# Optimization experiments

Hardware: AMD Instinct MI355X
Metric: run time of the kernel (lower is better)

Reference implementation:

```python
import jax, jax.numpy as jnp
import numpy as np

NUM_HEADS = 16

def _w8a8_linear(x_q, x_scale, w_q, w_scale, bias):
    # W8A8 GEMM with dynamic per-token input scale and per-output-channel weight scale
    # x_q: [N, Din] int8 values, w_q: [Dout, Din] int8 values
    acc = jnp.matmul(x_q.astype(jnp.float32), w_q.astype(jnp.float32).T)  # [N, Dout]
    return acc * (x_scale[:, None] * w_scale[None, :]) + bias[None, :]


def setup_inputs() -> dict:
    key = jax.random.key(0)
    ks = jax.random.split(key, 16)
    B, S, D = 2, 2048, 1024
    N = B * S
    def int8(k, shape):
        return jax.random.randint(k, shape, -127, 128, dtype=jnp.int32)
    inp = {
        "x_q": int8(ks[0], (N, D)),
        "x_scale": jax.random.uniform(ks[1], (N,), jnp.float32, 0.005, 0.02),
        "wq": int8(ks[2], (D, D)),
        "wq_scale": jax.random.uniform(ks[3], (D,), jnp.float32, 0.005, 0.02),
        "bq": jax.random.normal(ks[4], (D,), jnp.float32) * 0.02,
        "wk": int8(ks[5], (D, D)),
        "wk_scale": jax.random.uniform(ks[6], (D,), jnp.float32, 0.005, 0.02),
        "bk": jax.random.normal(ks[7], (D,), jnp.float32) * 0.02,
        "wv": int8(ks[8], (D, D)),
        "wv_scale": jax.random.uniform(ks[9], (D,), jnp.float32, 0.005, 0.02),
        "bv": jax.random.normal(ks[10], (D,), jnp.float32) * 0.02,
        "wo": int8(ks[11], (D, D)),
        "wo_scale": jax.random.uniform(ks[12], (D,), jnp.float32, 0.005, 0.02),
        "bo": jax.random.normal(ks[13], (D,), jnp.float32) * 0.02,
        "bsz": B,
        "qlen": S,
    }
    return inp


def reference(x_q, x_scale, wq, wq_scale, bq, wk, wk_scale, bk,
              wv, wv_scale, bv, wo, wo_scale, bo, bsz, qlen):
    D = wq.shape[0]
    hd = D // NUM_HEADS
    # quantized QKV projections (dequant fused into GEMM epilogue)
    q = _w8a8_linear(x_q, x_scale, wq, wq_scale, bq).reshape(bsz, qlen, NUM_HEADS, hd)
    k = _w8a8_linear(x_q, x_scale, wk, wk_scale, bk).reshape(bsz, qlen, NUM_HEADS, hd)
    v = _w8a8_linear(x_q, x_scale, wv, wv_scale, bv).reshape(bsz, qlen, NUM_HEADS, hd)
    # flash_attn_func(softmax_scale=None, causal=False) => scale = 1/sqrt(head_dim)
    scale = 1.0 / jnp.sqrt(jnp.float32(hd))
    scores = jnp.einsum('bqhd,bkhd->bhqk', q, k) * scale
    probs = jax.nn.softmax(scores, axis=-1)
    attn = jnp.einsum('bhqk,bkhd->bqhd', probs, v).reshape(bsz * qlen, D)
    # invoke_quant: dynamic per-token symmetric int8 quantization of attn output
    o_scale = jnp.max(jnp.abs(attn), axis=-1) / 127.0  # [N]
    o_q = jnp.clip(jnp.round(attn / o_scale[:, None]), -127.0, 127.0)
    # quantized out projection
    out = _w8a8_linear(o_q, o_scale, wo, wo_scale, bo)  # [N, D]
    return out
```

## Files before the change

kernel.cpp:

```cpp
#include <hip/hip_runtime.h>

#define D_MODEL 1024
#define NTOK    4096
#define SEQ     2048
#define NH      16
#define HD      64

typedef __bf16 bh8  __attribute__((ext_vector_type(8)));
typedef __bf16 bf4  __attribute__((ext_vector_type(4)));
typedef float  f32x4 __attribute__((ext_vector_type(4)));
typedef int    i32x4 __attribute__((ext_vector_type(4)));

__device__ __forceinline__ unsigned short f2bf(float f) {
  unsigned int u = __float_as_uint(f);
  u += 0x7fffu + ((u >> 16) & 1u);
  return (unsigned short)(u >> 16);
}
__device__ __forceinline__ float bf2f(unsigned short h) {
  return __uint_as_float(((unsigned int)h) << 16);
}
__device__ __forceinline__ float exp2a(float x) {
  float r; asm("v_exp_f32 %0, %1" : "=v"(r) : "v"(x)); return r;
}
__device__ __forceinline__ void gl16(const void* g, void* l) {
  __builtin_amdgcn_global_load_lds((const __attribute__((address_space(1))) unsigned int*)g,
                                   (__attribute__((address_space(3))) unsigned int*)l, 16, 0, 0);
}

__device__ __forceinline__ void pack_row(const int* src, unsigned* dst, int m, int t) {
  int4 w = *(const int4*)(src + (size_t)m * 1024 + t * 4);
  unsigned p01 = __builtin_amdgcn_perm((unsigned)w.y, (unsigned)w.x, 0x00000400u);
  unsigned p23 = __builtin_amdgcn_perm((unsigned)w.w, (unsigned)w.z, 0x00000400u);
  unsigned r   = __builtin_amdgcn_perm(p23, p01, 0x05040100u);
  int kg = t >> 4, c = (t >> 2) & 3, b4 = t & 3, sw = (m >> 1) & 3;
  dst[(size_t)m * 256 + kg * 16 + ((c ^ sw) << 2) + b4] = r;
}
__launch_bounds__(256)
__global__ void pack_x_k(const int* __restrict__ src, unsigned* __restrict__ dst) {
  pack_row(src, dst, blockIdx.x, threadIdx.x);
}
__launch_bounds__(256)
__global__ void pack_w_k(const int* __restrict__ s0, const int* __restrict__ s1,
                         const int* __restrict__ s2, const int* __restrict__ s3,
                         unsigned* __restrict__ d0, unsigned* __restrict__ d1,
                         unsigned* __restrict__ d2, unsigned* __restrict__ d3) {
  int wsel = blockIdx.x >> 10, m = blockIdx.x & 1023;
  const int* src = wsel == 0 ? s0 : wsel == 1 ? s1 : wsel == 2 ? s2 : s3;
  unsigned*  dst = wsel == 0 ? d0 : wsel == 1 ? d1 : wsel == 2 ? d2 : d3;
  pack_row(src, dst, m, threadIdx.x);
}

template <int MODE>
__launch_bounds__(256, 2)
__global__ void gemm8_k(const signed char* __restrict__ Ap, const signed char* __restrict__ Bp,
                        const float* __restrict__ sA, const float* __restrict__ sB,
                        const float* __restrict__ bias, float preScale, int kswz,
                        unsigned short* __restrict__ o1, unsigned short* __restrict__ o2,
                        float* __restrict__ outF)
{
  __shared__ __align__(16) signed char As[2][8192];
  __shared__ __align__(16) signed char Bs[2][8192];
  const int t = threadIdx.x, wid = t >> 6, lane = t & 63, g = lane >> 4, li = lane & 15;
  const int wm = wid >> 1, wn = wid & 1;
  const int m0 = blockIdx.y * 128, n0 = blockIdx.x * 128;

  i32x4 acc[4][4];
#pragma unroll
  for (int i = 0; i < 4; ++i)
#pragma unroll
    for (int j = 0; j < 4; ++j) acc[i][j] = (i32x4){0, 0, 0, 0};

  const int unitBase = wid * 2;
#pragma unroll
  for (int i = 0; i < 2; ++i) {
    int unit = (unitBase + i) * 64 + lane, r = unit >> 2, c = unit & 3;
    gl16(Ap + (size_t)(m0 + r) * 1024 + c * 16, (char*)As[0] + (unitBase + i) * 1024);
    gl16(Bp + (size_t)(n0 + r) * 1024 + c * 16, (char*)Bs[0] + (unitBase + i) * 1024);
  }
  __syncthreads();
  int p = 0;
#pragma unroll 1
  for (int ks = 0; ks < 16; ++ks) {
    if (ks < 15) {
      const int k0 = (ks + 1) * 64;
#pragma unroll
      for (int i = 0; i < 2; ++i) {
        int unit = (unitBase + i) * 64 + lane, r = unit >> 2, c = unit & 3;
        gl16(Ap + (size_t)(m0 + r) * 1024 + k0 + c * 16, (char*)As[p ^ 1] + (unitBase + i) * 1024);
        gl16(Bp + (size_t)(n0 + r) * 1024 + k0 + c * 16, (char*)Bs[p ^ 1] + (unitBase + i) * 1024);
      }
    }
    i32x4 af[4], bfr[4];
#pragma unroll
    for (int mt = 0; mt < 4; ++mt) {
      int row = wm * 64 + mt * 16 + li;
      af[mt] = *(const i32x4*)(As[p] + row * 64 + ((g ^ ((row >> 1) & 3)) << 4));
    }
#pragma unroll
    for (int nt = 0; nt < 4; ++nt) {
      int row = wn * 64 + nt * 16 + li;
      bfr[nt] = *(const i32x4*)(Bs[p] + row * 64 + ((g ^ ((row >> 1) & 3)) << 4));
    }
    __builtin_amdgcn_s_setprio(1);
#pragma unroll
    for (int mt = 0; mt < 4; ++mt)
#pragma unroll
      for (int nt = 0; nt < 4; ++nt)
        acc[mt][nt] = __builtin_amdgcn_mfma_i32_16x16x64_i8(af[mt], bfr[nt], acc[mt][nt], 0, 0, 0);
    __builtin_amdgcn_s_setprio(0);
    __syncthreads();
    p ^= 1;
  }

#pragma unroll
  for (int mt = 0; mt < 4; ++mt) {
#pragma unroll
    for (int nt = 0; nt < 4; ++nt) {
      const int nn = n0 + wn * 64 + nt * 16 + li;
#pragma unroll
      for (int r = 0; r < 4; ++r) {
        const int m = m0 + wm * 64 + mt * 16 + g * 4 + r;
        const float a = (float)acc[mt][nt][r];
        if (MODE == 0) {
          float f = (a * (sA[m] * sB[nn]) + bias[nn]) * preScale;
          int bb = m >> 11, s = m & 2047, hh = nn >> 6, d = nn & 63;
          int dd = kswz ? ((((d >> 3) ^ (s & 7)) << 3) | (d & 7)) : d;
          size_t o = (((size_t)(bb * NH + hh)) * SEQ + s) * HD + dd;
          unsigned short hi = f2bf(f);
          unsigned short lo = f2bf(f - bf2f(hi));
          o1[o] = hi; o2[o] = lo;
        } else if (MODE == 2) {
          float f = a * (sA[m] * sB[nn]) + bias[m];
          int hh = m >> 6, d = m & 63, bb = nn >> 11, s = nn & 2047;
          int ss = (s & ~63) | (((((s >> 3) & 7) ^ (d & 7)) << 3) | (s & 7));
          size_t o = (((size_t)(bb * NH + hh)) * HD + d) * SEQ + ss;
          o1[o] = f2bf(f);
        } else {
          outF[(size_t)m * 1024 + nn] = a * (sA[m] * sB[nn]) + bias[nn];
        }
      }
    }
  }
}

__launch_bounds__(256, 2)
__global__ void attn_k(const unsigned short* __restrict__ qhi, const unsigned short* __restrict__ qlo,
                       const unsigned short* __restrict__ khi, const unsigned short* __restrict__ klo,
                       const unsigned short* __restrict__ vt, float* __restrict__ attn)
{
  __shared__ __align__(16) unsigned short khs[64 * 64], kls[64 * 64], vts[64 * 64];
  __shared__ __align__(16) unsigned short ps[4][16 * 64];
  const int t = threadIdx.x;
  const int w = t >> 6, lane = t & 63, g = lane >> 4, li = lane & 15;
  const int q0 = blockIdx.x * 64, h = blockIdx.y, b = blockIdx.z;
  const int bh = b * NH + h;

  const unsigned short* qrh = qhi + ((size_t)bh * SEQ + q0 + w * 16 + li) * HD;
  const unsigned short* qrl = qlo + ((size_t)bh * SEQ + q0 + w * 16 + li) * HD;
  bh8 qhf[2], qlf[2];
#pragma unroll
  for (int kc = 0; kc < 2; ++kc) {
    qhf[kc] = *(const bh8*)(qrh + kc * 32 + g * 8);
    qlf[kc] = *(const bh8*)(qrl + kc * 32 + g * 8);
  }
  const unsigned short* kb = khi + (size_t)bh * SEQ * HD;
  const unsigned short* lb = klo + (size_t)bh * SEQ * HD;
  const unsigned short* vb = vt  + (size_t)bh * HD * SEQ;

  float m_run = -INFINITY, l_run = 0.0f;
  f32x4 ot[4];
#pragma unroll
  for (int i = 0; i < 4; ++i) ot[i] = (f32x4)0.0f;

  for (int kk0 = 0; kk0 < SEQ; kk0 += 64) {
    __syncthreads();
#pragma unroll
    for (int i = 0; i < 2; ++i) {
      int unit = (w * 2 + i) * 64 + lane, r = unit >> 3, c = unit & 7;
      gl16(kb + (size_t)(kk0 + r) * 64 + c * 8, (char*)khs + (w * 2 + i) * 1024);
      gl16(lb + (size_t)(kk0 + r) * 64 + c * 8, (char*)kls + (w * 2 + i) * 1024);
      gl16(vb + (size_t)r * SEQ + kk0 + c * 8, (char*)vts + (w * 2 + i) * 1024);
    }
    __syncthreads();

    f32x4 sa[4];
#pragma unroll
    for (int kt2 = 0; kt2 < 4; ++kt2) {
      sa[kt2] = (f32x4)0.0f;
      int row = kt2 * 16 + li, rx = row & 7;
#pragma unroll
      for (int kc = 0; kc < 2; ++kc) {
        bh8 kh = *(const bh8*)((const char*)khs + row * 128 + ((((kc << 2) | g) ^ rx) << 4));
        bh8 kl = *(const bh8*)((const char*)kls + row * 128 + ((((kc << 2) | g) ^ rx) << 4));
        __builtin_amdgcn_s_setprio(1);
        sa[kt2] = __builtin_amdgcn_mfma_f32_16x16x32_bf16(kh, qhf[kc], sa[kt2], 0, 0, 0);
        sa[kt2] = __builtin_amdgcn_mfma_f32_16x16x32_bf16(kh, qlf[kc], sa[kt2], 0, 0, 0);
        sa[kt2] = __builtin_amdgcn_mfma_f32_16x16x32_bf16(kl, qhf[kc], sa[kt2], 0, 0, 0);
        __builtin_amdgcn_s_setprio(0);
      }
    }
    float p[4][4];
    float sm = -INFINITY;
#pragma unroll
    for (int kt2 = 0; kt2 < 4; ++kt2)
#pragma unroll
      for (int r = 0; r < 4; ++r) { p[kt2][r] = sa[kt2][r]; sm = fmaxf(sm, p[kt2][r]); }
    sm = fmaxf(sm, __shfl_xor(sm, 16));
    sm = fmaxf(sm, __shfl_xor(sm, 32));
    if (__any(sm > m_run + 11.0f)) {
      float mn = fmaxf(m_run, sm);
      float alpha = exp2a(m_run - mn);
      l_run *= alpha;
#pragma unroll
      for (int i = 0; i < 4; ++i) ot[i] *= alpha;
      m_run = mn;
    }
    float ts = 0.0f;
#pragma unroll
    for (int kt2 = 0; kt2 < 4; ++kt2)
#pragma unroll
      for (int r = 0; r < 4; ++r) { float e = exp2a(p[kt2][r] - m_run); p[kt2][r] = e; ts += e; }
    ts += __shfl_xor(ts, 16);
    ts += __shfl_xor(ts, 32);
    l_run += ts;

#pragma unroll
    for (int kt2 = 0; kt2 < 4; ++kt2) {
      bf4 pk = { (__bf16)p[kt2][0], (__bf16)p[kt2][1], (__bf16)p[kt2][2], (__bf16)p[kt2][3] };
      int lchunk = (kt2 << 1) | (g >> 1);
      *(bf4*)((char*)ps[w] + li * 128 + ((lchunk ^ (li & 7)) << 4) + ((g & 1) << 3)) = pk;
    }
    asm volatile("s_waitcnt lgkmcnt(0)" ::: "memory");
    __builtin_amdgcn_sched_barrier(0);

#pragma unroll
    for (int kc2 = 0; kc2 < 2; ++kc2) {
      bh8 pf = *(const bh8*)((const char*)ps[w] + li * 128 + ((((kc2 << 2) | g) ^ (li & 7)) << 4));
#pragma unroll
      for (int dt = 0; dt < 4; ++dt) {
        int rowd = dt * 16 + li;
        bh8 vf = *(const bh8*)((const char*)vts + rowd * 128 + ((((kc2 << 2) | g) ^ (rowd & 7)) << 4));
        __builtin_amdgcn_s_setprio(1);
        ot[dt] = __builtin_amdgcn_mfma_f32_16x16x32_bf16(vf, pf, ot[dt], 0, 0, 0);
        __builtin_amdgcn_s_setprio(0);
      }
    }
  }

  const float inv = 1.0f / l_run;
  const int n = b * SEQ + q0 + w * 16 + li;
#pragma unroll
  for (int dt = 0; dt < 4; ++dt) {
    float4 o4;
    o4.x = ot[dt][0] * inv; o4.y = ot[dt][1] * inv;
    o4.z = ot[dt][2] * inv; o4.w = ot[dt][3] * inv;
    *(float4*)(attn + (size_t)n * D_MODEL + h * HD + dt * 16 + g * 4) = o4;
  }
}

__launch_bounds__(256)
__global__ void quant_k(const float* __restrict__ attn, unsigned* __restrict__ oqp,
                        float* __restrict__ osc)
{
  const int row = blockIdx.x, t = threadIdx.x;
  float4 v = *(const float4*)(attn + (size_t)row * D_MODEL + t * 4);
  float mx = fmaxf(fmaxf(fabsf(v.x), fabsf(v.y)), fmaxf(fabsf(v.z), fabsf(v.w)));
#pragma unroll
  for (int off = 1; off < 64; off <<= 1) mx = fmaxf(mx, __shfl_xor(mx, off));
  __shared__ float red[4];
  if ((t & 63) == 0) red[t >> 6] = mx;
  __syncthreads();
  mx = fmaxf(fmaxf(red[0], red[1]), fmaxf(red[2], red[3]));
  const float s = mx / 127.0f;
  if (t == 0) osc[row] = s;
  int q0 = (int)fminf(fmaxf(rintf(v.x / s), -127.f), 127.f);
  int q1 = (int)fminf(fmaxf(rintf(v.y / s), -127.f), 127.f);
  int q2 = (int)fminf(fmaxf(rintf(v.z / s), -127.f), 127.f);
  int q3 = (int)fminf(fmaxf(rintf(v.w / s), -127.f), 127.f);
  unsigned pk = ((unsigned)q0 & 255u) | (((unsigned)q1 & 255u) << 8) |
                (((unsigned)q2 & 255u) << 16) | (((unsigned)q3 & 255u) << 24);
  int kg = t >> 4, c = (t >> 2) & 3, b4 = t & 3, sw = (row >> 1) & 3;
  oqp[(size_t)row * 256 + kg * 16 + ((c ^ sw) << 2) + b4] = pk;
}

extern "C" void kernel_launch(void* const* d_in, const int* in_sizes, int n_in,
                              void* d_out, int out_size, void* d_ws, size_t ws_size,
                              hipStream_t stream)
{
  const int*   x   = (const int*)d_in[0];
  const float* xs  = (const float*)d_in[1];
  const int*   wq  = (const int*)d_in[2];
  const float* wqs = (const float*)d_in[3];
  const float* bq  = (const float*)d_in[4];
  const int*   wk  = (const int*)d_in[5];
  const float* wks = (const float*)d_in[6];
  const float* bk  = (const float*)d_in[7];
  const int*   wv  = (const int*)d_in[8];
  const float* wvs = (const float*)d_in[9];
  const float* bv  = (const float*)d_in[10];
  const int*   wo  = (const int*)d_in[11];
  const float* wos = (const float*)d_in[12];
  const float* bo  = (const float*)d_in[13];
  float* out = (float*)d_out;

  char* ws = (char*)d_ws;
  const size_t MB = 1024 * 1024;
  unsigned* xp  = (unsigned*)(ws);
  unsigned* wqp = (unsigned*)(ws + 4 * MB);
  unsigned* wkp = (unsigned*)(ws + 5 * MB);
  unsigned* wvp = (unsigned*)(ws + 6 * MB);
  unsigned* wop = (unsigned*)(ws + 7 * MB);
  unsigned short* qhi = (unsigned short*)(ws + 8 * MB);
  unsigned short* qlo = (unsigned short*)(ws + 16 * MB);
  unsigned short* khi = (unsigned short*)(ws + 24 * MB);
  unsigned short* klo = (unsigned short*)(ws + 32 * MB);
  unsigned short* vtw = (unsigned short*)(ws + 40 * MB);
  float*          att = (float*)(ws + 48 * MB);
  unsigned*       oqp = (unsigned*)(ws);
  float*          osc = (float*)(ws + 4 * MB);

  const float SC = 0.125f * 1.44269504088896340736f;
  dim3 blk(256);
  pack_x_k<<<dim3(4096), blk, 0, stream>>>(x, xp);
  pack_w_k<<<dim3(4096), blk, 0, stream>>>(wq, wk, wv, wo, wqp, wkp, wvp, wop);
  gemm8_k<0><<<dim3(8, 32), blk, 0, stream>>>((const signed char*)xp, (const signed char*)wqp,
                                              xs, wqs, bq, SC, 0, qhi, qlo, nullptr);
  gemm8_k<0><<<dim3(8, 32), blk, 0, stream>>>((const signed char*)xp, (const signed char*)wkp,
                                              xs, wks, bk, 1.0f, 1, khi, klo, nullptr);
  gemm8_k<2><<<dim3(32, 8), blk, 0, stream>>>((const signed char*)wvp, (const signed char*)xp,
                                              wvs, xs, bv, 1.0f, 0, vtw, nullptr, nullptr);
  attn_k<<<dim3(32, NH, 2), blk, 0, stream>>>(qhi, qlo, khi, klo, vtw, att);
  quant_k<<<dim3(4096), blk, 0, stream>>>(att, oqp, osc);
  gemm8_k<3><<<dim3(8, 32), blk, 0, stream>>>((const signed char*)oqp, (const signed char*)wop,
                                              osc, wos, bo, 1.0f, 0, nullptr, nullptr, out);
}
```

Before: 256.4 us.

## Merge QKV GEMMs into one launch, double-buffer K and widen attention tiles

The three QKV projection GEMMs become a single 768-block launch that picks the weight and epilogue from the block index. The output GEMM gets narrower 128x64 tiles so 512 blocks fill the device. The attention kernel now has each wave process two 16-query sub-tiles (128 queries per block), so each K/V tile is reused across more queries. K is double-buffered in LDS, and V is read straight from global memory into registers without its swizzle. This trades fewer launches and more reuse for higher register pressure and possibly less coalesced V loads.

```diff
diff --git a/kernel.cpp b/kernel.cpp
--- a/kernel.cpp
+++ b/kernel.cpp
@@ -50,19 +50,29 @@
   pack_row(src, dst, m, threadIdx.x);
 }
 
-template <int MODE>
 __launch_bounds__(256, 2)
-__global__ void gemm8_k(const signed char* __restrict__ Ap, const signed char* __restrict__ Bp,
-                        const float* __restrict__ sA, const float* __restrict__ sB,
-                        const float* __restrict__ bias, float preScale, int kswz,
-                        unsigned short* __restrict__ o1, unsigned short* __restrict__ o2,
-                        float* __restrict__ outF)
+__global__ void gemmQKV_k(const signed char* __restrict__ xp,
+                          const signed char* __restrict__ wqp,
+                          const signed char* __restrict__ wkp,
+                          const signed char* __restrict__ wvp,
+                          const float* __restrict__ xs,
+                          const float* __restrict__ wqs, const float* __restrict__ bq,
+                          const float* __restrict__ wks, const float* __restrict__ bk,
+                          const float* __restrict__ wvs, const float* __restrict__ bv,
+                          float SC,
+                          unsigned short* __restrict__ qhi, unsigned short* __restrict__ qlo,
+                          unsigned short* __restrict__ khi, unsigned short* __restrict__ klo,
+                          unsigned short* __restrict__ vtw)
 {
   __shared__ __align__(16) signed char As[2][8192];
   __shared__ __align__(16) signed char Bs[2][8192];
+  const int id = blockIdx.x, z = id >> 8, rb = id & 255;
   const int t = threadIdx.x, wid = t >> 6, lane = t & 63, g = lane >> 4, li = lane & 15;
   const int wm = wid >> 1, wn = wid & 1;
-  const int m0 = blockIdx.y * 128, n0 = blockIdx.x * 128;
+  const signed char *Ap, *Bp;
+  int m0, n0;
+  if (z == 2) { Ap = wvp; Bp = xp; m0 = (rb & 7) * 128; n0 = (rb >> 3) * 128; }
+  else        { Ap = xp; Bp = z ? wkp : wqp; m0 = (rb >> 3) * 128; n0 = (rb & 7) * 128; }
 
   i32x4 acc[4][4];
 #pragma unroll
@@ -121,26 +131,100 @@
       for (int r = 0; r < 4; ++r) {
         const int m = m0 + wm * 64 + mt * 16 + g * 4 + r;
         const float a = (float)acc[mt][nt][r];
-        if (MODE == 0) {
-          float f = (a * (sA[m] * sB[nn]) + bias[nn]) * preScale;
+        if (z == 2) {
+          float f = a * (wvs[m] * xs[nn]) + bv[m];
+          int hh = m >> 6, d = m & 63, bb = nn >> 11, s = nn & 2047;
+          size_t o = (((size_t)(bb * NH + hh)) * HD + d) * SEQ + s;
+          vtw[o] = f2bf(f);
+        } else {
+          const float* wsc = z ? wks : wqs;
+          const float* wbi = z ? bk : bq;
+          float f = (a * (xs[m] * wsc[nn]) + wbi[nn]) * (z ? 1.0f : SC);
           int bb = m >> 11, s = m & 2047, hh = nn >> 6, d = nn & 63;
-          int dd = kswz ? ((((d >> 3) ^ (s & 7)) << 3) | (d & 7)) : d;
+          int dd = z ? ((((d >> 3) ^ (s & 7)) << 3) | (d & 7)) : d;
           size_t o = (((size_t)(bb * NH + hh)) * SEQ + s) * HD + dd;
           unsigned short hi = f2bf(f);
           unsigned short lo = f2bf(f - bf2f(hi));
-          o1[o] = hi; o2[o] = lo;
-        } else if (MODE == 2) {
-          float f = a * (sA[m] * sB[nn]) + bias[m];
-          int hh = m >> 6, d = m & 63, bb = nn >> 11, s = nn & 2047;
-          int ss = (s & ~63) | (((((s >> 3) & 7) ^ (d & 7)) << 3) | (s & 7));
-          size_t o = (((size_t)(bb * NH + hh)) * HD + d) * SEQ + ss;
-          o1[o] = f2bf(f);
-        } else {
-          outF[(size_t)m * 1024 + nn] = a * (sA[m] * sB[nn]) + bias[nn];
+          if (z) { khi[o] = hi; klo[o] = lo; }
+          else   { qhi[o] = hi; qlo[o] = lo; }
         }
       }
     }
   }
+}
+
+__launch_bounds__(256, 2)
+__global__ void gemmO_k(const signed char* __restrict__ Ap, const signed char* __restrict__ Bp,
+                        const float* __restrict__ sA, const float* __restrict__ sB,
+                        const float* __restrict__ bias, float* __restrict__ outF)
+{
+  __shared__ __align__(16) signed char As[2][8192];
+  __shared__ __align__(16) signed char Bs[2][4096];
+  const int id = blockIdx.x;
+  const int m0 = (id >> 4) * 128, n0 = (id & 15) * 64;
+  const int t = threadIdx.x, wid = t >> 6, lane = t & 63, g = lane >> 4, li = lane & 15;
+  const int wm = wid >> 1, wn = wid & 1;
+
+  i32x4 acc[4][2];
+#pragma unroll
+  for (int i = 0; i < 4; ++i)
+#pragma unroll
+    for (int j = 0; j < 2; ++j) acc[i][j] = (i32x4){0, 0, 0, 0};
+
+#pragma unroll
+  for (int i = 0; i < 2; ++i) {
+    int unit = (wid * 2 + i) * 64 + lane, r = unit >> 2, c = unit & 3;
+    gl16(Ap + (size_t)(m0 + r) * 1024 + c * 16, (char*)As[0] + (wid * 2 + i) * 1024);
+  }
+  { int unit = wid * 64 + lane, r = unit >> 2, c = unit & 3;
+    gl16(Bp + (size_t)(n0 + r) * 1024 + c * 16, (char*)Bs[0] + wid * 1024); }
+  __syncthreads();
+  int p = 0;
+#pragma unroll 1
+  for (int ks = 0; ks < 16; ++ks) {
+    if (ks < 15) {
+      const int k0 = (ks + 1) * 64;
+#pragma unroll
+      for (int i = 0; i < 2; ++i) {
+        int unit = (wid * 2 + i) * 64 + lane, r = unit >> 2, c = unit & 3;
+        gl16(Ap + (size_t)(m0 + r) * 1024 + k0 + c * 16, (char*)As[p ^ 1] + (wid * 2 + i) * 1024);
+      }
+      { int unit = wid * 64 + lane, r = unit >> 2, c = unit & 3;
+        gl16(Bp + (size_t)(n0 + r) * 1024 + k0 + c * 16, (char*)Bs[p ^ 1] + wid * 1024); }
+    }
+    i32x4 af[4], bfr[2];
+#pragma unroll
+    for (int mt = 0; mt < 4; ++mt) {
+      int row = wm * 64 + mt * 16 + li;
+      af[mt] = *(const i32x4*)(As[p] + row * 64 + ((g ^ ((row >> 1) & 3)) << 4));
+    }
+#pragma unroll
+    for (int nt = 0; nt < 2; ++nt) {
+      int row = wn * 32 + nt * 16 + li;
+      bfr[nt] = *(const i32x4*)(Bs[p] + row * 64 + ((g ^ ((row >> 1) & 3)) << 4));
+    }
+    __builtin_amdgcn_s_setprio(1);
+#pragma unroll
+    for (int mt = 0; mt < 4; ++mt)
+#pragma unroll
+      for (int nt = 0; nt < 2; ++nt)
+        acc[mt][nt] = __builtin_amdgcn_mfma_i32_16x16x64_i8(af[mt], bfr[nt], acc[mt][nt], 0, 0, 0);
+    __builtin_amdgcn_s_setprio(0);
+    __syncthreads();
+    p ^= 1;
+  }
+
+#pragma unroll
+  for (int mt = 0; mt < 4; ++mt)
+#pragma unroll
+    for (int nt = 0; nt < 2; ++nt) {
+      const int nn = n0 + wn * 32 + nt * 16 + li;
+#pragma unroll
+      for (int r = 0; r < 4; ++r) {
+        const int m = m0 + wm * 64 + mt * 16 + g * 4 + r;
+        outF[(size_t)m * 1024 + nn] = (float)acc[mt][nt][r] * (sA[m] * sB[nn]) + bias[nn];
+      }
+    }
 }
 
 __launch_bounds__(256, 2)
@@ -148,113 +232,147 @@
                        const unsigned short* __restrict__ khi, const unsigned short* __restrict__ klo,
                        const unsigned short* __restrict__ vt, float* __restrict__ attn)
 {
-  __shared__ __align__(16) unsigned short khs[64 * 64], kls[64 * 64], vts[64 * 64];
-  __shared__ __align__(16) unsigned short ps[4][16 * 64];
+  __shared__ __align__(16) unsigned short khs[2][4096], kls[2][4096];
+  __shared__ __align__(16) unsigned short ps[4][2][1024];
   const int t = threadIdx.x;
   const int w = t >> 6, lane = t & 63, g = lane >> 4, li = lane & 15;
-  const int q0 = blockIdx.x * 64, h = blockIdx.y, b = blockIdx.z;
+  const int q0 = blockIdx.x * 128, h = blockIdx.y, b = blockIdx.z;
   const int bh = b * NH + h;
-
-  const unsigned short* qrh = qhi + ((size_t)bh * SEQ + q0 + w * 16 + li) * HD;
-  const unsigned short* qrl = qlo + ((size_t)bh * SEQ + q0 + w * 16 + li) * HD;
-  bh8 qhf[2], qlf[2];
+  const int qA = q0 + w * 32 + li, qB = qA + 16;
+
+  bh8 qhf[2][2], qlf[2][2];
 #pragma unroll
   for (int kc = 0; kc < 2; ++kc) {
-    qhf[kc] = *(const bh8*)(qrh + kc * 32 + g * 8);
-    qlf[kc] = *(const bh8*)(qrl + kc * 32 + g * 8);
+    qhf[0][kc] = *(const bh8*)(qhi + ((size_t)bh * SEQ + qA) * HD + kc * 32 + g * 8);
+    qlf[0][kc] = *(const bh8*)(qlo + ((size_t)bh * SEQ + qA) * HD + kc * 32 + g * 8);
+    qhf[1][kc] = *(const bh8*)(qhi + ((size_t)bh * SEQ + qB) * HD + kc * 32 + g * 8);
+    qlf[1][kc] = *(const bh8*)(qlo + ((size_t)bh * SEQ + qB) * HD + kc * 32 + g * 8);
   }
   const unsigned short* kb = khi + (size_t)bh * SEQ * HD;
   const unsigned short* lb = klo + (size_t)bh * SEQ * HD;
   const unsigned short* vb = vt  + (size_t)bh * HD * SEQ;
 
-  float m_run = -INFINITY, l_run = 0.0f;
-  f32x4 ot[4];
-#pragma unroll
-  for (int i = 0; i < 4; ++i) ot[i] = (f32x4)0.0f;
-
-  for (int kk0 = 0; kk0 < SEQ; kk0 += 64) {
+  float m_run[2] = {-INFINITY, -INFINITY}, l_run[2] = {0.0f, 0.0f};
+  f32x4 ot[2][4];
+#pragma unroll
+  for (int s = 0; s < 2; ++s)
+#pragma unroll
+    for (int i = 0; i < 4; ++i) ot[s][i] = (f32x4)0.0f;
+
+#pragma unroll
+  for (int i = 0; i < 2; ++i) {
+    int unit = (w * 2 + i) * 64 + lane, r = unit >> 3, c = unit & 7;
+    gl16(kb + (size_t)r * 64 + c * 8, (char*)khs[0] + (w * 2 + i) * 1024);
+    gl16(lb + (size_t)r * 64 + c * 8, (char*)kls[0] + (w * 2 + i) * 1024);
+  }
+
+#pragma unroll 1
+  for (int it = 0; it < 32; ++it) {
+    const int kk0 = it * 64, cur = it & 1;
     __syncthreads();
-#pragma unroll
-    for (int i = 0; i < 2; ++i) {
-      int unit = (w * 2 + i) * 64 + lane, r = unit >> 3, c = unit & 7;
-      gl16(kb + (size_t)(kk0 + r) * 64 + c * 8, (char*)khs + (w * 2 + i) * 1024);
-      gl16(lb + (size_t)(kk0 + r) * 64 + c * 8, (char*)kls + (w * 2 + i) * 1024);
-      gl16(vb + (size_t)r * SEQ + kk0 + c * 8, (char*)vts + (w * 2 + i) * 1024);
-    }
-    __syncthreads();
-
-    f32x4 sa[4];
+    bh8 vreg[2][4];
+#pragma unroll
+    for (int kc2 = 0; kc2 < 2; ++kc2)
+#pragma unroll
+      for (int dt = 0; dt < 4; ++dt)
+        vreg[kc2][dt] = *(const bh8*)(vb + (size_t)(dt * 16 + li) * SEQ + kk0 + kc2 * 32 + g * 8);
+    if (it < 31) {
+#pragma unroll
+      for (int i = 0; i < 2; ++i) {
+        int unit = (w * 2 + i) * 64 + lane, r = unit >> 3, c = unit & 7;
+        gl16(kb + (size_t)(kk0 + 64 + r) * 64 + c * 8, (char*)khs[cur ^ 1] + (w * 2 + i) * 1024);
+        gl16(lb + (size_t)(kk0 + 64 + r) * 64 + c * 8, (char*)kls[cur ^ 1] + (w * 2 + i) * 1024);
+      }
+    }
+    f32x4 sa[2][4];
+#pragma unroll
+    for (int s = 0; s < 2; ++s)
+#pragma unroll
+      for (int i = 0; i < 4; ++i) sa[s][i] = (f32x4)0.0f;
 #pragma unroll
     for (int kt2 = 0; kt2 < 4; ++kt2) {
-      sa[kt2] = (f32x4)0.0f;
       int row = kt2 * 16 + li, rx = row & 7;
 #pragma unroll
       for (int kc = 0; kc < 2; ++kc) {
-        bh8 kh = *(const bh8*)((const char*)khs + row * 128 + ((((kc << 2) | g) ^ rx) << 4));
-        bh8 kl = *(const bh8*)((const char*)kls + row * 128 + ((((kc << 2) | g) ^ rx) << 4));
+        bh8 kh = *(const bh8*)((const char*)khs[cur] + row * 128 + ((((kc << 2) | g) ^ rx) << 4));
+        bh8 kl = *(const bh8*)((const char*)kls[cur] + row * 128 + ((((kc << 2) | g) ^ rx) << 4));
         __builtin_amdgcn_s_setprio(1);
-        sa[kt2] = __builtin_amdgcn_mfma_f32_16x16x32_bf16(kh, qhf[kc], sa[kt2], 0, 0, 0);
-        sa[kt2] = __builtin_amdgcn_mfma_f32_16x16x32_bf16(kh, qlf[kc], sa[kt2], 0, 0, 0);
-        sa[kt2] = __builtin_amdgcn_mfma_f32_16x16x32_bf16(kl, qhf[kc], sa[kt2], 0, 0, 0);
+        sa[0][kt2] = __builtin_amdgcn_mfma_f32_16x16x32_bf16(kh, qhf[0][kc], sa[0][kt2], 0, 0, 0);
+        sa[1][kt2] = __builtin_amdgcn_mfma_f32_16x16x32_bf16(kh, qhf[1][kc], sa[1][kt2], 0, 0, 0);
+        sa[0][kt2] = __builtin_amdgcn_mfma_f32_16x16x32_bf16(kh, qlf[0][kc], sa[0][kt2], 0, 0, 0);
+        sa[1][kt2] = __builtin_amdgcn_mfma_f32_16x16x32_bf16(kh, qlf[1][kc], sa[1][kt2], 0, 0, 0);
+        sa[0][kt2] = __builtin_amdgcn_mfma_f32_16x16x32_bf16(kl, qhf[0][kc], sa[0][kt2], 0, 0, 0);
+        sa[1][kt2] = __builtin_amdgcn_mfma_f32_16x16x32_bf16(kl, qhf[1][kc], sa[1][kt2], 0, 0, 0);
         __builtin_amdgcn_s_setprio(0);
       }
     }
-    float p[4][4];
-    float sm = -INFINITY;
-#pragma unroll
-    for (int kt2 = 0; kt2 < 4; ++kt2)
-#pragma unroll
-      for (int r = 0; r < 4; ++r) { p[kt2][r] = sa[kt2][r]; sm = fmaxf(sm, p[kt2][r]); }
-    sm = fmaxf(sm, __shfl_xor(sm, 16));
-    sm = fmaxf(sm, __shfl_xor(sm, 32));
-    if (__any(sm > m_run + 11.0f)) {
-      float mn = fmaxf(m_run, sm);
-      float alpha = exp2a(m_run - mn);
-      l_run *= alpha;
-#pragma unroll
-      for (int i = 0; i < 4; ++i) ot[i] *= alpha;
-      m_run = mn;
-    }
-    float ts = 0.0f;
-#pragma unroll
-    for (int kt2 = 0; kt2 < 4; ++kt2)
-#pragma unroll
-      for (int r = 0; r < 4; ++r) { float e = exp2a(p[kt2][r] - m_run); p[kt2][r] = e; ts += e; }
-    ts += __shfl_xor(ts, 16);
-    ts += __shfl_xor(ts, 32);
-    l_run += ts;
-
-#pragma unroll
-    for (int kt2 = 0; kt2 < 4; ++kt2) {
-      bf4 pk = { (__bf16)p[kt2][0], (__bf16)p[kt2][1], (__bf16)p[kt2][2], (__bf16)p[kt2][3] };
-      int lchunk = (kt2 << 1) | (g >> 1);
-      *(bf4*)((char*)ps[w] + li * 128 + ((lchunk ^ (li & 7)) << 4) + ((g & 1) << 3)) = pk;
+#pragma unroll
+    for (int s = 0; s < 2; ++s) {
+      float sm = -INFINITY;
+#pragma unroll
+      for (int kt2 = 0; kt2 < 4; ++kt2)
+#pragma unroll
+        for (int r = 0; r < 4; ++r) sm = fmaxf(sm, sa[s][kt2][r]);
+      sm = fmaxf(sm, __shfl_xor(sm, 16));
+      sm = fmaxf(sm, __shfl_xor(sm, 32));
+      if (__any(sm > m_run[s] + 11.0f)) {
+        float mn = fmaxf(m_run[s], sm);
+        float alpha = exp2a(m_run[s] - mn);
+        l_run[s] *= alpha;
+#pragma unroll
+        for (int i = 0; i < 4; ++i) ot[s][i] *= alpha;
+        m_run[s] = mn;
+      }
+      float ts = 0.0f;
+#pragma unroll
+      for (int kt2 = 0; kt2 < 4; ++kt2)
+#pragma unroll
+        for (int r = 0; r < 4; ++r) {
+          float e = exp2a(sa[s][kt2][r] - m_run[s]);
+          sa[s][kt2][r] = e; ts += e;
+        }
+      ts += __shfl_xor(ts, 16);
+      ts += __shfl_xor(ts, 32);
+      l_run[s] += ts;
+#pragma unroll
+      for (int kt2 = 0; kt2 < 4; ++kt2) {
+        bf4 pk = { (__bf16)sa[s][kt2][0], (__bf16)sa[s][kt2][1],
+                   (__bf16)sa[s][kt2][2], (__bf16)sa[s][kt2][3] };
+        int lchunk = (kt2 << 1) | (g >> 1);
+        *(bf4*)((char*)ps[w][s] + li * 128 + ((lchunk ^ (li & 7)) << 4) + ((g & 1) << 3)) = pk;
+      }
     }
     asm volatile("s_waitcnt lgkmcnt(0)" ::: "memory");
     __builtin_amdgcn_sched_barrier(0);
-
+    bh8 pf[2][2];
+#pragma unroll
+    for (int s = 0; s < 2; ++s)
+#pragma unroll
+      for (int kc2 = 0; kc2 < 2; ++kc2)
+        pf[s][kc2] = *(const bh8*)((const char*)ps[w][s] + li * 128 + ((((kc2 << 2) | g) ^ (li & 7)) << 4));
 #pragma unroll
     for (int kc2 = 0; kc2 < 2; ++kc2) {
-      bh8 pf = *(const bh8*)((const char*)ps[w] + li * 128 + ((((kc2 << 2) | g) ^ (li & 7)) << 4));
+      __builtin_amdgcn_s_setprio(1);
 #pragma unroll
       for (int dt = 0; dt < 4; ++dt) {
-        int rowd = dt * 16 + li;
-        bh8 vf = *(const bh8*)((const char*)vts + rowd * 128 + ((((kc2 << 2) | g) ^ (rowd & 7)) << 4));
-        __builtin_amdgcn_s_setprio(1);
-        ot[dt] = __builtin_amdgcn_mfma_f32_16x16x32_bf16(vf, pf, ot[dt], 0, 0, 0);
-        __builtin_amdgcn_s_setprio(0);
-      }
-    }
-  }
-
-  const float inv = 1.0f / l_run;
-  const int n = b * SEQ + q0 + w * 16 + li;
-#pragma unroll
-  for (int dt = 0; dt < 4; ++dt) {
-    float4 o4;
-    o4.x = ot[dt][0] * inv; o4.y = ot[dt][1] * inv;
-    o4.z = ot[dt][2] * inv; o4.w = ot[dt][3] * inv;
-    *(float4*)(attn + (size_t)n * D_MODEL + h * HD + dt * 16 + g * 4) = o4;
+        ot[0][dt] = __builtin_amdgcn_mfma_f32_16x16x32_bf16(vreg[kc2][dt], pf[0][kc2], ot[0][dt], 0, 0, 0);
+        ot[1][dt] = __builtin_amdgcn_mfma_f32_16x16x32_bf16(vreg[kc2][dt], pf[1][kc2], ot[1][dt], 0, 0, 0);
+      }
+      __builtin_amdgcn_s_setprio(0);
+    }
+  }
+
+#pragma unroll
+  for (int s = 0; s < 2; ++s) {
+    const float inv = 1.0f / l_run[s];
+    const int n = b * SEQ + (s ? qB : qA);
+#pragma unroll
+    for (int dt = 0; dt < 4; ++dt) {
+      float4 o4;
+      o4.x = ot[s][dt][0] * inv; o4.y = ot[s][dt][1] * inv;
+      o4.z = ot[s][dt][2] * inv; o4.w = ot[s][dt][3] * inv;
+      *(float4*)(attn + (size_t)n * D_MODEL + h * HD + dt * 16 + g * 4) = o4;
+    }
   }
 }
 
@@ -323,14 +441,12 @@
   dim3 blk(256);
   pack_x_k<<<dim3(4096), blk, 0, stream>>>(x, xp);
   pack_w_k<<<dim3(4096), blk, 0, stream>>>(wq, wk, wv, wo, wqp, wkp, wvp, wop);
-  gemm8_k<0><<<dim3(8, 32), blk, 0, stream>>>((const signed char*)xp, (const signed char*)wqp,
-                                              xs, wqs, bq, SC, 0, qhi, qlo, nullptr);
-  gemm8_k<0><<<dim3(8, 32), blk, 0, stream>>>((const signed char*)xp, (const signed char*)wkp,
-                                              xs, wks, bk, 1.0f, 1, khi, klo, nullptr);
-  gemm8_k<2><<<dim3(32, 8), blk, 0, stream>>>((const signed char*)wvp, (const signed char*)xp,
-                                              wvs, xs, bv, 1.0f, 0, vtw, nullptr, nullptr);
-  attn_k<<<dim3(32, NH, 2), blk, 0, stream>>>(qhi, qlo, khi, klo, vtw, att);
+  gemmQKV_k<<<dim3(768), blk, 0, stream>>>((const signed char*)xp, (const signed char*)wqp,
+                                           (const signed char*)wkp, (const signed char*)wvp,
+                                           xs, wqs, bq, wks, bk, wvs, bv, SC,
+                                           qhi, qlo, khi, klo, vtw);
+  attn_k<<<dim3(16, NH, 2), blk, 0, stream>>>(qhi, qlo, khi, klo, vtw, att);
   quant_k<<<dim3(4096), blk, 0, stream>>>(att, oqp, osc);
-  gemm8_k<3><<<dim3(8, 32), blk, 0, stream>>>((const signed char*)oqp, (const signed char*)wop,
-                                              osc, wos, bo, 1.0f, 0, nullptr, nullptr, out);
-}
+  gemmO_k<<<dim3(512), blk, 0, stream>>>((const signed char*)oqp, (const signed char*)wop,
+                                         osc, wos, bo, out);
+}
```

New measurement: 258.4 us. About the same (+0.8%).
